# Optimization experiments

Hardware: AMD Instinct MI355X
Metric: run time of the kernel (lower is better)

The kernel has to match this reference:

```python
import jax, jax.numpy as jnp
import numpy as np

FEATURE_SIZE = 100000
FIELD_SIZE = 39
EMBED_SIZE = 16
BATCH = 4096


def setup_inputs() -> dict:
    key = jax.random.key(0)
    k1, k2, k3, k4 = jax.random.split(key, 4)
    feature_idx = jax.random.randint(k1, (BATCH, FIELD_SIZE), 0, FEATURE_SIZE)
    feature_values = jax.random.uniform(k2, (BATCH, FIELD_SIZE), dtype=jnp.float32)
    feature_embeddings = jax.random.normal(
        k3, (FEATURE_SIZE, FIELD_SIZE, EMBED_SIZE), dtype=jnp.float32)
    weights_first_order = jax.random.normal(k4, (FEATURE_SIZE, 1), dtype=jnp.float32)
    fm_bias = jnp.zeros((1,), dtype=jnp.float32)
    return {
        "feature_idx": feature_idx,
        "feature_values": feature_values,
        "feature_embeddings": feature_embeddings,
        "weights_first_order": weights_first_order,
        "fm_bias": fm_bias,
    }


def reference(feature_idx, feature_values, feature_embeddings, weights_first_order, fm_bias):
    # First order: gather per-feature scalar weights -> [B, F]
    w1 = weights_first_order[feature_idx, 0]
    first_order = jnp.sum(feature_values * w1, axis=1, keepdims=True)  # [B,1]

    # Field-aware gather: E[b, i, f, :] = feature_embeddings[idx[b,i], f, :]
    E = feature_embeddings[feature_idx]  # [B, F, F, E]

    # S[b,i,j] = <v_{i,fj}, v_{j,fi}>  (dot over embedding dim)
    S = jnp.einsum('bije,bjie->bij', E, E)  # [B, F, F]

    vv = feature_values[:, :, None] * feature_values[:, None, :]  # [B, F, F]
    F = feature_idx.shape[1]
    upper = jnp.triu(jnp.ones((F, F), dtype=bool), k=1)  # i < j pairs
    second_order = jnp.sum(jnp.where(upper, S * vv, 0.0), axis=(1, 2))[:, None]  # [B,1]

    return second_order + first_order + fm_bias
```

## Files before the change

kernel.cpp:

```cpp
#include <hip/hip_runtime.h>
#include <hip/hip_fp16.h>

#define BATCH 4096
#define FIELD 39
#define EMBED 16
#define ROW_F4 (FIELD * EMBED / 4)
#define TOT_F4 (FIELD * ROW_F4)
#define NPAIRS (FIELD * (FIELD - 1))
#define NTASK2 (NPAIRS * 2)
#define BLOCK 1024
#define NWAVES (BLOCK / 64)
#define SITER ((TOT_F4 + BLOCK - 1) / BLOCK)
#define CITER ((NTASK2 + BLOCK - 1) / BLOCK)

__global__ __launch_bounds__(BLOCK, 8) void ffm_kernel(
    const int*   __restrict__ idx,
    const float* __restrict__ vals,
    const float* __restrict__ emb,
    const float* __restrict__ w1,
    const float* __restrict__ bias,
    float*       __restrict__ out)
{
    const int b   = blockIdx.x;
    const int tid = threadIdx.x;

    __shared__ __align__(16) __half s_emb[FIELD * FIELD * EMBED];
    __shared__ int    s_idx[FIELD];
    __shared__ float  s_val[FIELD];
    __shared__ float  s_red[NWAVES];

    if (tid < FIELD) {
        s_idx[tid] = idx[b * FIELD + tid];
        s_val[tid] = vals[b * FIELD + tid];
    }
    __syncthreads();

    const float4* emb4 = (const float4*)emb;
    float4 g[SITER];
    #pragma unroll
    for (int it = 0; it < SITER; ++it) {
        int t  = tid + it * BLOCK;
        int tc = t < TOT_F4 ? t : TOT_F4 - 1;
        int i  = tc / ROW_F4;
        int off = tc - i * ROW_F4;
        g[it] = emb4[s_idx[i] * ROW_F4 + off];
    }

    float acc = 0.0f;
    if (tid < FIELD) {
        acc = s_val[tid] * w1[s_idx[tid]];
    }

    __half2* s2 = (__half2*)s_emb;
    #pragma unroll
    for (int it = 0; it < SITER; ++it) {
        int t = tid + it * BLOCK;
        if (t < TOT_F4) {
            s2[t * 2]     = __floats2half2_rn(g[it].x, g[it].y);
            s2[t * 2 + 1] = __floats2half2_rn(g[it].z, g[it].w);
        }
    }
    __syncthreads();

    #pragma unroll
    for (int it = 0; it < CITER; ++it) {
        int t = tid + it * BLOCK;
        if (t < NTASK2) {
            int p = t >> 1;
            int h = t & 1;
            int i = p / (FIELD - 1);
            int r = p - i * (FIELD - 1);
            int j = r + (r >= i ? 1 : 0);
            float4 av = *(const float4*)&s_emb[(i * FIELD + j) * EMBED + h * 8];
            float4 cv = *(const float4*)&s_emb[(j * FIELD + i) * EMBED + h * 8];
            const __half2* ah = (const __half2*)&av;
            const __half2* ch = (const __half2*)&cv;
            float dot = 0.0f;
            #pragma unroll
            for (int k = 0; k < 4; ++k) {
                float2 a = __half22float2(ah[k]);
                float2 c = __half22float2(ch[k]);
                dot += a.x * c.x + a.y * c.y;
            }
            acc += dot * (0.5f * s_val[i] * s_val[j]);
        }
    }

    #pragma unroll
    for (int off = 32; off > 0; off >>= 1)
        acc += __shfl_down(acc, off, 64);

    const int wave = tid >> 6;
    const int lane = tid & 63;
    if (lane == 0) s_red[wave] = acc;
    __syncthreads();

    if (tid == 0) {
        float s = 0.0f;
        #pragma unroll
        for (int w = 0; w < NWAVES; ++w) s += s_red[w];
        out[b] = s + bias[0];
    }
}

extern "C" void kernel_launch(void* const* d_in, const int* in_sizes, int n_in,
                              void* d_out, int out_size, void* d_ws, size_t ws_size,
                              hipStream_t stream) {
    const int*   idx  = (const int*)d_in[0];
    const float* vals = (const float*)d_in[1];
    const float* emb  = (const float*)d_in[2];
    const float* w1   = (const float*)d_in[3];
    const float* bias = (const float*)d_in[4];
    float* out = (float*)d_out;

    ffm_kernel<<<BATCH, BLOCK, 0, stream>>>(idx, vals, emb, w1, bias, out);
}
```

Baseline: 345.5 us.

## Pad shared embedding rows, drop index staging sync, prescale values

Each gathered embedding row in LDS is padded from 624 to 632 halves so the strided cross reads (j,i) land in different LDS banks. The initial shared-memory staging of indices and its __syncthreads are removed, so gather addresses read idx straight from global memory. Feature values are prescaled by 1/sqrt(2), which removes the 0.5 multiply in the pair loop. The trade-off is slightly more LDS per block and repeated global idx loads, which are cached.

```diff
diff --git a/kernel.cpp b/kernel.cpp
--- a/kernel.cpp
+++ b/kernel.cpp
@@ -13,6 +13,9 @@
 #define SITER ((TOT_F4 + BLOCK - 1) / BLOCK)
 #define CITER ((NTASK2 + BLOCK - 1) / BLOCK)
 
+#define ROW_H 632
+#define ROW_H2 (ROW_H / 2)
+
 __global__ __launch_bounds__(BLOCK, 8) void ffm_kernel(
     const int*   __restrict__ idx,
     const float* __restrict__ vals,
@@ -24,16 +27,9 @@
     const int b   = blockIdx.x;
     const int tid = threadIdx.x;
 
-    __shared__ __align__(16) __half s_emb[FIELD * FIELD * EMBED];
-    __shared__ int    s_idx[FIELD];
+    __shared__ __align__(16) __half s_emb[FIELD * ROW_H];
     __shared__ float  s_val[FIELD];
     __shared__ float  s_red[NWAVES];
-
-    if (tid < FIELD) {
-        s_idx[tid] = idx[b * FIELD + tid];
-        s_val[tid] = vals[b * FIELD + tid];
-    }
-    __syncthreads();
 
     const float4* emb4 = (const float4*)emb;
     float4 g[SITER];
@@ -42,13 +38,15 @@
         int t  = tid + it * BLOCK;
         int tc = t < TOT_F4 ? t : TOT_F4 - 1;
         int i  = tc / ROW_F4;
-        int off = tc - i * ROW_F4;
-        g[it] = emb4[s_idx[i] * ROW_F4 + off];
+        int o  = tc - i * ROW_F4;
+        g[it] = emb4[idx[b * FIELD + i] * ROW_F4 + o];
     }
 
     float acc = 0.0f;
     if (tid < FIELD) {
-        acc = s_val[tid] * w1[s_idx[tid]];
+        float v = vals[b * FIELD + tid];
+        s_val[tid] = v * 0.70710678118654752f;
+        acc = v * w1[idx[b * FIELD + tid]];
     }
 
     __half2* s2 = (__half2*)s_emb;
@@ -56,8 +54,11 @@
     for (int it = 0; it < SITER; ++it) {
         int t = tid + it * BLOCK;
         if (t < TOT_F4) {
-            s2[t * 2]     = __floats2half2_rn(g[it].x, g[it].y);
-            s2[t * 2 + 1] = __floats2half2_rn(g[it].z, g[it].w);
+            int i  = t / ROW_F4;
+            int o  = t - i * ROW_F4;
+            int p2 = i * ROW_H2 + o * 2;
+            s2[p2]     = __floats2half2_rn(g[it].x, g[it].y);
+            s2[p2 + 1] = __floats2half2_rn(g[it].z, g[it].w);
         }
     }
     __syncthreads();
@@ -71,8 +72,8 @@
             int i = p / (FIELD - 1);
             int r = p - i * (FIELD - 1);
             int j = r + (r >= i ? 1 : 0);
-            float4 av = *(const float4*)&s_emb[(i * FIELD + j) * EMBED + h * 8];
-            float4 cv = *(const float4*)&s_emb[(j * FIELD + i) * EMBED + h * 8];
+            float4 av = *(const float4*)&s_emb[i * ROW_H + j * EMBED + h * 8];
+            float4 cv = *(const float4*)&s_emb[j * ROW_H + i * EMBED + h * 8];
             const __half2* ah = (const __half2*)&av;
             const __half2* ch = (const __half2*)&cv;
             float dot = 0.0f;
@@ -82,7 +83,7 @@
                 float2 c = __half22float2(ch[k]);
                 dot += a.x * c.x + a.y * c.y;
             }
-            acc += dot * (0.5f * s_val[i] * s_val[j]);
+            acc += dot * (s_val[i] * s_val[j]);
         }
     }
 
```

After: 344.4 us. No clear change (-0.3%).
